# Optimization experiments

Measured on AMD Instinct MI355X. Metric: run time of the kernel, lower is better.

## Reference

```python
import jax, jax.numpy as jnp
import numpy as np

B, IN_DIM, HID = 8192, 1024, 1024

def setup_inputs() -> dict:
    key = jax.random.key(0)
    ks = jax.random.split(key, 11)
    s_in = 1.0 / np.sqrt(IN_DIM + HID)  # torch Linear default init scale
    inp = {
        "Z": jax.random.normal(ks[0], (B, IN_DIM), dtype=jnp.float32),
        "h_prev": jax.random.normal(ks[1], (B, HID), dtype=jnp.float32),
        "c_prev": jax.random.normal(ks[2], (B, HID), dtype=jnp.float32),
        "W_i": jax.random.uniform(ks[3], (IN_DIM + HID, HID), jnp.float32, -s_in, s_in),
        "b_i": jax.random.uniform(ks[4], (HID,), jnp.float32, -s_in, s_in),
        "W_f": jax.random.uniform(ks[5], (IN_DIM + HID, HID), jnp.float32, -s_in, s_in),
        "b_f": jax.random.uniform(ks[6], (HID,), jnp.float32, -s_in, s_in),
        "W_o": jax.random.uniform(ks[7], (IN_DIM + HID, HID), jnp.float32, -s_in, s_in),
        "b_o": jax.random.uniform(ks[8], (HID,), jnp.float32, -s_in, s_in),
        "W_g": jax.random.uniform(ks[9], (IN_DIM + HID, HID), jnp.float32, -s_in, s_in),
        "b_g": jax.random.uniform(ks[10], (HID,), jnp.float32, -s_in, s_in),
    }
    return inp

def reference(Z, h_prev, c_prev, W_i, b_i, W_f, b_f, W_o, b_o, W_g, b_g):
    combined = jnp.concatenate([Z, h_prev], axis=1)  # [B, IN+HID]
    i = jax.nn.sigmoid(combined @ W_i + b_i)
    f = jax.nn.sigmoid(combined @ W_f + b_f)
    o = jax.nn.sigmoid(combined @ W_o + b_o)
    g = jnp.tanh(combined @ W_g + b_g)
    c = f * c_prev + i * g
    h = o * jnp.tanh(c)
    return (h, c)
```

## Files before the change

kernel.cpp:

```cpp
#include <hip/hip_runtime.h>


#define BDIM 8192
#define KDIM 2048
#define NDIM 1024
#define NCAT 4096
#define NT   32

typedef __bf16 bf16x8 __attribute__((ext_vector_type(8)));
typedef __bf16 bf16x4 __attribute__((ext_vector_type(4)));
typedef float  f32x4  __attribute__((ext_vector_type(4)));

__device__ __forceinline__ void async_cp16(const void* g, void* l) {
    __builtin_amdgcn_global_load_lds((__attribute__((address_space(1))) void*)g,
                                     (__attribute__((address_space(3))) void*)l,
                                     16, 0, 0);
}

__device__ __forceinline__ float sigm(float x) { return 1.f / (1.f + __expf(-x)); }
__device__ __forceinline__ float tanh_fast(float x) { return 1.f - 2.f / (1.f + __expf(2.f * x)); }

#define BARM asm volatile("s_barrier" ::: "memory")

__global__ __launch_bounds__(256)
void prep_kernel(const float* __restrict__ Z, const float* __restrict__ H,
                 const float* __restrict__ Wi, const float* __restrict__ Wf,
                 const float* __restrict__ Wo, const float* __restrict__ Wg,
                 __bf16* __restrict__ A, __bf16* __restrict__ Wt) {
    __shared__ float t[64][65];
    const int bid = blockIdx.x;
    const int tid = threadIdx.x;

    if (bid < 8192) {
        const bool isZ = (bid < 4096);
        const int idx  = (isZ ? bid : bid - 4096) * 256 + tid;
        const int row  = idx >> 7;
        const int q8   = idx & 127;
        const float* src = isZ ? Z : H;
        const float4* p = (const float4*)src + ((size_t)row << 8) + q8 * 2;
        float4 v0 = p[0], v1 = p[1];
        bf16x8 o = { (__bf16)v0.x, (__bf16)v0.y, (__bf16)v0.z, (__bf16)v0.w,
                     (__bf16)v1.x, (__bf16)v1.y, (__bf16)v1.z, (__bf16)v1.w };
        const int col8 = isZ ? q8 : (q8 + 128);
        ((bf16x8*)A)[(size_t)row * 256 + col8] = o;
    } else {
        const int id  = bid - 8192;
        const int g   = id >> 9;
        const int rem = id & 511;
        const int k0  = (rem & 31) * 64;
        const int n0  = (rem >> 5) * 64;
        const float* W = (g == 0) ? Wi : (g == 1) ? Wf : (g == 2) ? Wo : Wg;

        const int c4 = tid & 15, r0 = tid >> 4;
        #pragma unroll
        for (int it = 0; it < 4; ++it) {
            const int r = r0 + it * 16;
            float4 v = ((const float4*)W)[(size_t)(k0 + r) * 256 + (n0 >> 2) + c4];
            t[r][c4 * 4 + 0] = v.x;
            t[r][c4 * 4 + 1] = v.y;
            t[r][c4 * 4 + 2] = v.z;
            t[r][c4 * 4 + 3] = v.w;
        }
        __syncthreads();

        const int kc = tid & 7, nn0 = tid >> 3;
        #pragma unroll
        for (int j = 0; j < 2; ++j) {
            const int n    = nn0 + j * 32;
            const int ncat = n0 + n;
            const size_t outRow = (size_t)(ncat >> 5) * 128 + g * 32 + (ncat & 31);
            bf16x8 o;
            #pragma unroll
            for (int kk = 0; kk < 8; ++kk) o[kk] = (__bf16)t[kc * 8 + kk][n];
            *(bf16x8*)(Wt + outRow * KDIM + k0 + kc * 8) = o;
        }
    }
}

__global__ __launch_bounds__(512, 2)
void lstm_gemm_kernel(const __bf16* __restrict__ A, const __bf16* __restrict__ Wt,
                      const float* __restrict__ b_i, const float* __restrict__ b_f,
                      const float* __restrict__ b_o, const float* __restrict__ b_g,
                      const float* __restrict__ c_prev, float* __restrict__ out) {
    extern __shared__ char smem[];

    const int tid  = threadIdx.x;
    const int wave = tid >> 6;
    const int lane = tid & 63;
    const int wm   = wave >> 2;
    const int wn   = wave & 3;
    const int l15  = lane & 15;
    const int quad = lane >> 4;

    const int bid = blockIdx.x;
    const int bxc = (bid & 7) * 2 + (bid >> 8);
    const int by  = (bid >> 3) & 31;
    const int m0   = by * 256;
    const int cat0 = bxc * 256;
    const int n0   = bxc * 64;

    const int grow   = wave * 8 + (lane >> 3);
    const int schunk = (lane & 7) ^ (((lane >> 5) & 1) << 1);
    const __bf16* Ags = A  + (size_t)(m0   + grow) * KDIM + schunk * 8;
    const __bf16* Bgs = Wt + (size_t)(cat0 + grow) * KDIM + schunk * 8;
    char* ldsw = smem + wave * 1024;

#define STG(o, h, kt, b) do { \
    const __bf16* gp_ = ((o) ? Bgs : Ags) + (size_t)(h) * 128 * KDIM + (size_t)(kt) * 64; \
    char* lp_ = ldsw + (b) * 65536 + (o) * 32768 + (h) * 16384; \
    async_cp16(gp_, lp_); \
    async_cp16(gp_ + (size_t)64 * KDIM, lp_ + 8192); \
} while (0)

    const int xorr = ((l15 >> 2) & 1) << 1;
    const int cA0  = (quad ^ xorr) * 16;
    const int cA1  = ((quad + 4) ^ xorr) * 16;
    const int aoff0 = wm * 16384 + l15 * 128;
    const int boff0 = 32768 + (wn >> 1) * 16384 + ((wn & 1) * 64 + l15) * 128;

    f32x4 acc[8][4];
    #pragma unroll
    for (int i = 0; i < 8; ++i)
        #pragma unroll
        for (int j = 0; j < 4; ++j) acc[i][j] = (f32x4){0.f, 0.f, 0.f, 0.f};

    bf16x8 af[4][2];
    bf16x8 bf[4][2];

    auto LDA = [&](int mh, int bufb) {
        const char* p = smem + bufb + aoff0 + mh * 8192;
        #pragma unroll
        for (int m = 0; m < 4; ++m) {
            af[m][0] = *(const bf16x8*)(p + m * 2048 + cA0);
            af[m][1] = *(const bf16x8*)(p + m * 2048 + cA1);
        }
    };
    auto LDB = [&](int nh, int bufb) {
        const char* p = smem + bufb + boff0 + nh * 4096;
        #pragma unroll
        for (int n = 0; n < 2; ++n) {
            bf[nh * 2 + n][0] = *(const bf16x8*)(p + n * 2048 + cA0);
            bf[nh * 2 + n][1] = *(const bf16x8*)(p + n * 2048 + cA1);
        }
    };
    auto MMA = [&](int mh, int nh) {
        #pragma unroll
        for (int m = 0; m < 4; ++m)
            #pragma unroll
            for (int n = 0; n < 2; ++n) {
                acc[mh * 4 + m][nh * 2 + n] = __builtin_amdgcn_mfma_f32_16x16x32_bf16(
                    af[m][0], bf[nh * 2 + n][0], acc[mh * 4 + m][nh * 2 + n], 0, 0, 0);
                acc[mh * 4 + m][nh * 2 + n] = __builtin_amdgcn_mfma_f32_16x16x32_bf16(
                    af[m][1], bf[nh * 2 + n][1], acc[mh * 4 + m][nh * 2 + n], 0, 0, 0);
            }
    };

    STG(0, 0, 0, 0); STG(1, 0, 0, 0); STG(0, 1, 0, 0); STG(1, 1, 0, 0);
    STG(0, 0, 1, 1); STG(1, 0, 1, 1);
    asm volatile("s_waitcnt vmcnt(4)" ::: "memory");
    BARM;

    #pragma unroll 2
    for (int t = 0; t < NT; ++t) {
        const int b    = t & 1;
        const int bufb = b * 65536;
        LDA(0, bufb); LDB(0, bufb);
        if (t + 1 < NT) STG(0, 1, t + 1, b ^ 1);
        BARM; asm volatile("s_waitcnt lgkmcnt(0)" ::: "memory");
        __builtin_amdgcn_s_setprio(1); MMA(0, 0); __builtin_amdgcn_s_setprio(0);
        BARM;
        LDB(1, bufb);
        if (t + 1 < NT) STG(1, 1, t + 1, b ^ 1);
        BARM; asm volatile("s_waitcnt lgkmcnt(0)" ::: "memory");
        __builtin_amdgcn_s_setprio(1); MMA(0, 1); __builtin_amdgcn_s_setprio(0);
        BARM;
        LDA(1, bufb);
        BARM; asm volatile("s_waitcnt lgkmcnt(0)" ::: "memory");
        __builtin_amdgcn_s_setprio(1); MMA(1, 0); __builtin_amdgcn_s_setprio(0);
        BARM;
        if (t + 2 < NT) { STG(0, 0, t + 2, b); STG(1, 0, t + 2, b); }
        if (t < NT - 2) { asm volatile("s_waitcnt vmcnt(4)" ::: "memory"); }
        else            { asm volatile("s_waitcnt vmcnt(0)" ::: "memory"); }
        BARM;
        __builtin_amdgcn_s_setprio(1); MMA(1, 1); __builtin_amdgcn_s_setprio(0);
        BARM;
    }

    float* Ep = (float*)smem;
    const int nn = tid & 63;
    const float bvi = b_i[n0 + nn], bvf = b_f[n0 + nn];
    const float bvo = b_o[n0 + nn], bvg = b_g[n0 + nn];
    int colW[4];
    #pragma unroll
    for (int nt = 0; nt < 4; ++nt)
        colW[nt] = ((wn & 1) * 2 + (nt >> 1)) * 64 + (wn >> 1) * 32 + (nt & 1) * 16 + l15;

    #pragma unroll
    for (int ch = 0; ch < 4; ++ch) {
        BARM;
        if (wm == (ch >> 1)) {
            #pragma unroll
            for (int mi = 0; mi < 4; ++mi) {
                const int mt = (ch & 1) * 4 + mi;
                #pragma unroll
                for (int nt = 0; nt < 4; ++nt)
                    #pragma unroll
                    for (int r = 0; r < 4; ++r)
                        Ep[(mi * 16 + quad * 4 + r) * 258 + colW[nt]] = acc[mt][nt][r];
            }
        }
        BARM;
        #pragma unroll
        for (int e = 0; e < 8; ++e) {
            const int row = e * 8 + wave;
            const float gi = sigm(Ep[row * 258 + nn] + bvi);
            const float gf = sigm(Ep[row * 258 + 64 + nn] + bvf);
            const float go = sigm(Ep[row * 258 + 128 + nn] + bvo);
            const float gg = tanh_fast(Ep[row * 258 + 192 + nn] + bvg);
            const size_t pos = (size_t)(m0 + ch * 64 + row) * NDIM + n0 + nn;
            const float cp = c_prev[pos];
            const float cv = gf * cp + gi * gg;
            out[pos] = go * tanh_fast(cv);
            out[(size_t)BDIM * NDIM + pos] = cv;
        }
    }
#undef STG
}

extern "C" void kernel_launch(void* const* d_in, const int* in_sizes, int n_in,
                              void* d_out, int out_size, void* d_ws, size_t ws_size,
                              hipStream_t stream) {
    const float* Z  = (const float*)d_in[0];
    const float* H  = (const float*)d_in[1];
    const float* Cp = (const float*)d_in[2];
    const float* Wi = (const float*)d_in[3];
    const float* bi = (const float*)d_in[4];
    const float* Wf = (const float*)d_in[5];
    const float* bf = (const float*)d_in[6];
    const float* Wo = (const float*)d_in[7];
    const float* bo = (const float*)d_in[8];
    const float* Wg = (const float*)d_in[9];
    const float* bg = (const float*)d_in[10];

    __bf16* Acomb = (__bf16*)d_ws;
    __bf16* Wt    = (__bf16*)((char*)d_ws + (size_t)33554432);

    static bool cfg = false;
    if (!cfg) {
        hipFuncSetAttribute(reinterpret_cast<const void*>(lstm_gemm_kernel),
                            hipFuncAttributeMaxDynamicSharedMemorySize, 131072);
        cfg = true;
    }

    prep_kernel<<<10240, 256, 0, stream>>>(Z, H, Wi, Wf, Wo, Wg, Acomb, Wt);
    lstm_gemm_kernel<<<512, 512, 131072, stream>>>(
        Acomb, Wt, bi, bf, bo, bg, Cp, (float*)d_out);
}
```

Measured before the change: 324.8 us.

## Restage LDS tiles as two 32-wide K halves with new swizzle

Changes how global-to-LDS async copies map threads to rows and K chunks. Each thread now loads four 16-byte chunks of a 64-byte row half, and the two copies cover the two 32-element K halves placed 8 KB apart instead of rows 64 apart. The LDS read addressing and XOR swizzle are rewritten to match, aiming for more contiguous global accesses per wave and fewer LDS bank conflicts. The epilogue barriers become __syncthreads, which adds full memory fences around the epilogue staging.

```diff
diff --git a/kernel.cpp b/kernel.cpp
--- a/kernel.cpp
+++ b/kernel.cpp
@@ -8,7 +8,6 @@
 #define NT   32
 
 typedef __bf16 bf16x8 __attribute__((ext_vector_type(8)));
-typedef __bf16 bf16x4 __attribute__((ext_vector_type(4)));
 typedef float  f32x4  __attribute__((ext_vector_type(4)));
 
 __device__ __forceinline__ void async_cp16(const void* g, void* l) {
@@ -99,24 +98,22 @@
     const int cat0 = bxc * 256;
     const int n0   = bxc * 64;
 
-    const int grow   = wave * 8 + (lane >> 3);
-    const int schunk = (lane & 7) ^ (((lane >> 5) & 1) << 1);
-    const __bf16* Ags = A  + (size_t)(m0   + grow) * KDIM + schunk * 8;
-    const __bf16* Bgs = Wt + (size_t)(cat0 + grow) * KDIM + schunk * 8;
+    const int srow = tid >> 2;
+    const int sgch = (tid & 3) ^ ((tid >> 3) & 3);
+    const __bf16* Ags = A  + (size_t)(m0   + srow) * KDIM + sgch * 8;
+    const __bf16* Bgs = Wt + (size_t)(cat0 + srow) * KDIM + sgch * 8;
     char* ldsw = smem + wave * 1024;
 
 #define STG(o, h, kt, b) do { \
-    const __bf16* gp_ = ((o) ? Bgs : Ags) + (size_t)(h) * 128 * KDIM + (size_t)(kt) * 64; \
+    const __bf16* gp_ = ((o) ? Bgs : Ags) + (size_t)(h) * 128 * KDIM + (kt) * 64; \
     char* lp_ = ldsw + (b) * 65536 + (o) * 32768 + (h) * 16384; \
-    async_cp16(gp_, lp_); \
-    async_cp16(gp_ + (size_t)64 * KDIM, lp_ + 8192); \
+    async_cp16(gp_,      lp_); \
+    async_cp16(gp_ + 32, lp_ + 8192); \
 } while (0)
 
-    const int xorr = ((l15 >> 2) & 1) << 1;
-    const int cA0  = (quad ^ xorr) * 16;
-    const int cA1  = ((quad + 4) ^ xorr) * 16;
-    const int aoff0 = wm * 16384 + l15 * 128;
-    const int boff0 = 32768 + (wn >> 1) * 16384 + ((wn & 1) * 64 + l15) * 128;
+    const int swz   = (quad ^ ((l15 >> 1) & 3)) * 16;
+    const int abase = wm * 16384 + l15 * 64 + swz;
+    const int bbase = 32768 + (wn >> 1) * 16384 + ((wn & 1) * 64 + l15) * 64 + swz;
 
     f32x4 acc[8][4];
     #pragma unroll
@@ -128,19 +125,19 @@
     bf16x8 bf[4][2];
 
     auto LDA = [&](int mh, int bufb) {
-        const char* p = smem + bufb + aoff0 + mh * 8192;
+        const char* p = smem + bufb + abase + mh * 4096;
         #pragma unroll
         for (int m = 0; m < 4; ++m) {
-            af[m][0] = *(const bf16x8*)(p + m * 2048 + cA0);
-            af[m][1] = *(const bf16x8*)(p + m * 2048 + cA1);
+            af[m][0] = *(const bf16x8*)(p + m * 1024);
+            af[m][1] = *(const bf16x8*)(p + m * 1024 + 8192);
         }
     };
     auto LDB = [&](int nh, int bufb) {
-        const char* p = smem + bufb + boff0 + nh * 4096;
+        const char* p = smem + bufb + bbase + nh * 2048;
         #pragma unroll
         for (int n = 0; n < 2; ++n) {
-            bf[nh * 2 + n][0] = *(const bf16x8*)(p + n * 2048 + cA0);
-            bf[nh * 2 + n][1] = *(const bf16x8*)(p + n * 2048 + cA1);
+            bf[nh * 2 + n][0] = *(const bf16x8*)(p + n * 1024);
+            bf[nh * 2 + n][1] = *(const bf16x8*)(p + n * 1024 + 8192);
         }
     };
     auto MMA = [&](int mh, int nh) {
@@ -197,7 +194,7 @@
 
     #pragma unroll
     for (int ch = 0; ch < 4; ++ch) {
-        BARM;
+        __syncthreads();
         if (wm == (ch >> 1)) {
             #pragma unroll
             for (int mi = 0; mi < 4; ++mi) {
@@ -209,7 +206,7 @@
                         Ep[(mi * 16 + quad * 4 + r) * 258 + colW[nt]] = acc[mt][nt][r];
             }
         }
-        BARM;
+        __syncthreads();
         #pragma unroll
         for (int e = 0; e < 8; ++e) {
             const int row = e * 8 + wave;
```

Measured after the change: 319.7 us. About the same (-1.6%).
